# Optimization experiments

Hardware: AMD Instinct MI355X
Metric: run time of the kernel (lower is better)

## Reference

```python
import jax, jax.numpy as jnp
import numpy as np

B, N, M, D, V = 16, 2048, 2048, 128, 128


def setup_inputs() -> dict:
    key0 = jax.random.key(0)
    kq, kk, kv, kp = jax.random.split(key0, 4)
    return {
        "query": jax.random.normal(kq, (B, N, D), dtype=jnp.float32),
        "key": jax.random.normal(kk, (B, M, D), dtype=jnp.float32),
        "value": jax.random.normal(kv, (B, M, V), dtype=jnp.float32),
        "key_padding_len": jax.random.randint(kp, (B,), 0, 512),
        "is_attn_mask_len": 1,  # Python int -> causal masking on
    }


def reference(query, key, value, key_padding_len, is_attn_mask_len):
    # query:[B,N,D], key:[B,M,D], value:[B,M,V], key_padding_len:[B]
    Bq, Nq, Dq = query.shape
    Mk = key.shape[1]
    scale = 1.0 / jnp.sqrt(jnp.asarray(Dq, dtype=query.dtype))

    # torch mask(): zero out the LAST key_padding_len key positions
    pos = jnp.arange(Mk)
    keep = pos[None, :] < (Mk - key_padding_len)[:, None]  # [B,M]
    key = jnp.where(keep[:, :, None], key, jnp.zeros((), key.dtype))

    score = jnp.einsum("bnd,bmd->bnm", query, key) * scale  # [B,N,M]

    if is_attn_mask_len:
        # attn_mask_len[b,i] = M-1-i  ->  row i keeps positions j <= i (causal)
        causal = pos[None, :] <= jnp.arange(Nq)[:, None]  # [N,M]
        score = jnp.where(causal[None, :, :], score, jnp.asarray(-1e6, score.dtype))

    attn = jax.nn.softmax(score, axis=-1)  # dropout p=0 -> identity
    out = jnp.einsum("bnm,bmv->bnv", attn, value)  # [B,N,V]
    return out
```

## Files before the change

### kernel.cpp

```cpp
#include <hip/hip_runtime.h>
#include <stdint.h>

typedef unsigned short ushort_t;
typedef __attribute__((ext_vector_type(8))) short short8;
typedef __attribute__((ext_vector_type(4))) float floatx4;

#define SEQ_N 2048
#define SEQ_M 2048
#define DIM_D 128
#define DIM_V 128
#define BC 64
#define BC2 32


#if __has_builtin(__builtin_amdgcn_exp2f)
#define EXP2F(x) __builtin_amdgcn_exp2f(x)
#else
#define EXP2F(x) exp2f(x)
#endif

template <int CTRL>
__device__ __forceinline__ float dpp_f(float x) {
  int xi = __builtin_bit_cast(int, x);
  int yi = __builtin_amdgcn_update_dpp(xi, xi, CTRL, 0xf, 0xf, false);
  return __builtin_bit_cast(float, yi);
}
__device__ __forceinline__ float rowmax16(float x) {
  x = fmaxf(x, dpp_f<0x128>(x));
  x = fmaxf(x, dpp_f<0x124>(x));
  x = fmaxf(x, dpp_f<0x122>(x));
  x = fmaxf(x, dpp_f<0x121>(x));
  return x;
}
__device__ __forceinline__ float rowsum16(float x) {
  x += dpp_f<0x128>(x);
  x += dpp_f<0x124>(x);
  x += dpp_f<0x122>(x);
  x += dpp_f<0x121>(x);
  return x;
}

__device__ __forceinline__ ushort_t f2bf(float f) {
  uint32_t u = __builtin_bit_cast(uint32_t, f);
  return (ushort_t)((u + 0x8000u) >> 16);
}
__device__ __forceinline__ uint32_t bfpack(float lo, float hi) {
  uint32_t a = __builtin_bit_cast(uint32_t, lo) + 0x8000u;
  uint32_t b = __builtin_bit_cast(uint32_t, hi) + 0x8000u;
  return __builtin_amdgcn_perm(b, a, 0x07060302u);
}

#define K2OFF 0
#define V2OFF 8192
#define P2OFF 16384
#define SMEM2 18432
#define KELEMS 4096
#define VELEMS 4096

#define WS2_KB 0
#define WS2_VT 2097152
#define WS2_PO 4194304
#define WS2_M  8388608
#define WS2_L  8454144
#define WS2_FLOATS 8519680

__device__ __forceinline__ void stage16(const ushort_t* src, ushort_t* lds_base, int lane) {
#if __has_builtin(__builtin_amdgcn_global_load_lds)
  __builtin_amdgcn_global_load_lds(
      (const __attribute__((address_space(1))) void*)src,
      (__attribute__((address_space(3))) void*)lds_base, 16, 0, 0);
#else
  *(uint4*)(lds_base + lane * 8) = *(const uint4*)src;
#endif
}

__global__ __launch_bounds__(256)
void prep2(const float* __restrict__ K, const float* __restrict__ Vg,
           const int* __restrict__ kpl, float* __restrict__ ws) {
  __shared__ __align__(16) ushort_t lt[64][72];
  ushort_t* Kb = (ushort_t*)(ws + WS2_KB);
  ushort_t* Vt = (ushort_t*)(ws + WS2_VT);
  const int g = blockIdx.x, tid = threadIdx.x;
  if (g < 2048) {
    const size_t e = (size_t)g * 2048 + (size_t)tid * 8;
    const int row = (int)(e >> 7);
    const int b = row >> 11, mm = row & 2047;
    const int mlimit = SEQ_M - kpl[b];
    uint4 kw = make_uint4(0u, 0u, 0u, 0u);
    if (mm < mlimit) {
      const float* p = K + e;
      float4 f0 = *(const float4*)p, f1 = *(const float4*)(p + 4);
      kw.x = bfpack(f0.x, f0.y); kw.y = bfpack(f0.z, f0.w);
      kw.z = bfpack(f1.x, f1.y); kw.w = bfpack(f1.z, f1.w);
    }
    *(uint4*)(Kb + e) = kw;
  } else {
    const int g2 = g - 2048;
    const int b = g2 >> 6;
    const int mt = (g2 & 63) >> 1;
    const int vh = (g2 & 1) * 64;
    const int mrow = tid >> 2, v0 = (tid & 3) * 16;
    const float* p = Vg + ((size_t)b * SEQ_M + (size_t)(mt * 64 + mrow)) * DIM_V + vh + v0;
    float4 f0 = *(const float4*)p, f1 = *(const float4*)(p + 4);
    float4 f2 = *(const float4*)(p + 8), f3 = *(const float4*)(p + 12);
    lt[v0 +  0][mrow] = f2bf(f0.x); lt[v0 +  1][mrow] = f2bf(f0.y);
    lt[v0 +  2][mrow] = f2bf(f0.z); lt[v0 +  3][mrow] = f2bf(f0.w);
    lt[v0 +  4][mrow] = f2bf(f1.x); lt[v0 +  5][mrow] = f2bf(f1.y);
    lt[v0 +  6][mrow] = f2bf(f1.z); lt[v0 +  7][mrow] = f2bf(f1.w);
    lt[v0 +  8][mrow] = f2bf(f2.x); lt[v0 +  9][mrow] = f2bf(f2.y);
    lt[v0 + 10][mrow] = f2bf(f2.z); lt[v0 + 11][mrow] = f2bf(f2.w);
    lt[v0 + 12][mrow] = f2bf(f3.x); lt[v0 + 13][mrow] = f2bf(f3.y);
    lt[v0 + 14][mrow] = f2bf(f3.z); lt[v0 + 15][mrow] = f2bf(f3.w);
    __syncthreads();
    const int v = tid >> 2, mo = (tid & 3) * 16;
    ushort_t* dst = Vt + ((size_t)(b * DIM_V + vh + v) * SEQ_M) + mt * 64 + mo;
    *(uint4*)(dst + 0) = *(const uint4*)&lt[v][mo];
    *(uint4*)(dst + 8) = *(const uint4*)&lt[v][mo + 8];
  }
}

__global__ __launch_bounds__(256, 4)
void fa2(const float* __restrict__ Q, const int* __restrict__ amask,
         float* __restrict__ Out, float* __restrict__ ws) {
  __shared__ __align__(16) ushort_t sm[SMEM2];
  const ushort_t* __restrict__ Kb = (const ushort_t*)(ws + WS2_KB);
  const ushort_t* __restrict__ Vt = (const ushort_t*)(ws + WS2_VT);

  const int tid = threadIdx.x;
  const int lane = tid & 63;
  const int w = tid >> 6;
  const int qd = lane >> 4;
  const int nn = lane & 15;

  const int bx = blockIdx.x;
  const int xcd = bx & 7;
  const int q8 = bx >> 3;
  const int s  = q8 >> 5;
  const int v  = q8 & 31;
  const int p  = v & 1;
  const int j  = v >> 1;
  const int b  = xcd * 2 + p;
  const int jj = p ? (15 - j) : j;
  int rt, c;
  if (s == 0)      { rt = jj;      c = 0; }
  else if (s == 1) { rt = 31 - jj; c = 0; }
  else if (s == 2) { rt = 16 + jj; c = 1; }
  else             { rt = 15 - jj; c = 1; }

  const int flag = amask[0];
  const int ntf = flag ? (2 * rt + 2) : (SEQ_M / BC2);
  const int sp  = flag ? (rt + 1) : (SEQ_M / BC2 / 2);
  const int jt_lo = c ? sp : 0;
  const int jt_hi = c ? ntf : sp;

  const int i0w = rt * 64 + w * 16;
  const float c1 = 0.08838834764831845f * 1.4426950408889634f;

  short8 qf[4];
  {
    const float* Qb = Q + ((size_t)b * SEQ_N + (size_t)(i0w + nn)) * DIM_D;
    union { short8 v; uint32_t u32[4]; } tq;
#pragma unroll
    for (int ks = 0; ks < 4; ++ks) {
      const float* pq = Qb + ks * 32 + qd * 8;
      float4 f0 = *(const float4*)pq, f1 = *(const float4*)(pq + 4);
      tq.u32[0] = bfpack(f0.x, f0.y);
      tq.u32[1] = bfpack(f0.z, f0.w);
      tq.u32[2] = bfpack(f1.x, f1.y);
      tq.u32[3] = bfpack(f1.z, f1.w);
      qf[ks] = tq.v;
    }
  }

  floatx4 o[8];
#pragma unroll
  for (int vt = 0; vt < 8; ++vt) o[vt] = (floatx4)0.0f;
  float m[4], l[4];
#pragma unroll
  for (int r = 0; r < 4; ++r) { m[r] = -3.0e38f; l[r] = 0.0f; }

  const size_t kbatch = (size_t)b * (SEQ_M * DIM_D);
  const size_t vbatch = (size_t)b * ((size_t)DIM_V * SEQ_M);

  auto stage = [&](int buf, int jt) {
    const int jb = jt * BC2;
#pragma unroll
    for (int i = 0; i < 2; ++i) {
      const int seg = w * 2 + i;
      {
        const int rrow = seg * 4 + (lane >> 4);
        const int col  = ((lane & 15) * 8) ^ ((rrow & 7) << 3);
        const ushort_t* src = Kb + kbatch + ((size_t)(jb + rrow) << 7) + col;
        stage16(src, &sm[K2OFF + buf * KELEMS + seg * 512], lane);
      }
      {
        const int vrow = seg * 16 + (lane >> 2);
        const int colg = (lane & 3) ^ ((lane >> 4) & 3);
        const ushort_t* src = Vt + vbatch + ((size_t)vrow << 11) + jb + colg * 8;
        stage16(src, &sm[V2OFF + buf * VELEMS + seg * 512], lane);
      }
    }
  };

  stage(0, jt_lo);
  __syncthreads();

  const int len = jt_hi - jt_lo;
  const int swl = (nn & 7) << 3;
  const int vsw = ((nn >> 2) & 3) << 3;
#pragma unroll 1
  for (int t = 0; t < len; ++t) {
    const int cur = t & 1;
    const int jbase = (jt_lo + t) * BC2;
    if (t + 1 < len) stage(cur ^ 1, jt_lo + t + 1);

    const int kb = K2OFF + cur * KELEMS;
    const int vb = V2OFF + cur * VELEMS;

    floatx4 sx[2];
#pragma unroll
    for (int ct = 0; ct < 2; ++ct) sx[ct] = (floatx4)0.0f;
    __builtin_amdgcn_s_setprio(1);
#pragma unroll
    for (int ks = 0; ks < 4; ++ks) {
#pragma unroll
      for (int ct = 0; ct < 2; ++ct) {
        short8 bf = *(const short8*)&sm[kb + (ct * 16 + nn) * 128
                                        + ((ks * 32 + qd * 8) ^ swl)];
        sx[ct] = __builtin_amdgcn_mfma_f32_16x16x32_bf16(qf[ks], bf, sx[ct], 0, 0, 0);
      }
    }
    __builtin_amdgcn_s_setprio(0);

    {
      const bool needmask = flag && (jbase + BC2 - 1 > i0w);
      if (needmask) {
#pragma unroll
        for (int ct = 0; ct < 2; ++ct) {
          const int jgl = jbase + ct * 16 + nn;
#pragma unroll
          for (int r = 0; r < 4; ++r) {
            float tv = sx[ct][r] * c1;
            sx[ct][r] = (jgl > i0w + qd * 4 + r) ? -3.0e38f : tv;
          }
        }
      } else {
#pragma unroll
        for (int ct = 0; ct < 2; ++ct)
#pragma unroll
          for (int r = 0; r < 4; ++r) sx[ct][r] *= c1;
      }
      float mr4[4];
#pragma unroll
      for (int r = 0; r < 4; ++r) mr4[r] = rowmax16(fmaxf(sx[0][r], sx[1][r]));
      bool need = false;
#pragma unroll
      for (int r = 0; r < 4; ++r) need = need || (mr4[r] > m[r] + 8.0f);
      if (__any(need ? 1 : 0)) {
#pragma unroll
        for (int r = 0; r < 4; ++r) {
          const float mn = fmaxf(m[r], mr4[r]);
          const float alpha = EXP2F(m[r] - mn);
          m[r] = mn;
          l[r] *= alpha;
#pragma unroll
          for (int vt = 0; vt < 8; ++vt) o[vt][r] *= alpha;
        }
      }
#pragma unroll
      for (int r = 0; r < 4; ++r) {
        const int prow = w * 16 + qd * 4 + r;
        float p0 = EXP2F(sx[0][r] - m[r]);
        float p1 = EXP2F(sx[1][r] - m[r]);
        l[r] += p0 + p1;
        sm[P2OFF + prow * 32 + ((0 * 16 + nn) ^ (qd << 3))] = f2bf(p0);
        sm[P2OFF + prow * 32 + ((1 * 16 + nn) ^ (qd << 3))] = f2bf(p1);
      }
    }

    __builtin_amdgcn_s_setprio(1);
    {
      short8 a = *(const short8*)&sm[P2OFF + (w * 16 + nn) * 32 + ((qd * 8) ^ vsw)];
#pragma unroll
      for (int vt = 0; vt < 8; ++vt) {
        short8 vbf = *(const short8*)&sm[vb + (vt * 16 + nn) * 32 + ((qd * 8) ^ vsw)];
        o[vt] = __builtin_amdgcn_mfma_f32_16x16x32_bf16(a, vbf, o[vt], 0, 0, 0);
      }
    }
    __builtin_amdgcn_s_setprio(0);

    __syncthreads();
  }

#pragma unroll
  for (int r = 0; r < 4; ++r) l[r] = rowsum16(l[r]);

  const int rb = b * 32 + rt;
  if (c == 0) {
    float* Od = Out + ((size_t)b * SEQ_N + i0w) * DIM_V;
#pragma unroll
    for (int r = 0; r < 4; ++r) {
      const int row = qd * 4 + r;
#pragma unroll
      for (int vt = 0; vt < 8; ++vt)
        Od[(size_t)row * DIM_V + vt * 16 + nn] = o[vt][r];
    }
  } else {
    float* Od = ws + WS2_PO + (size_t)rb * (64 * DIM_V);
#pragma unroll
    for (int r = 0; r < 4; ++r) {
      const int row = w * 16 + qd * 4 + r;
#pragma unroll
      for (int vt = 0; vt < 8; ++vt)
        Od[(size_t)row * DIM_V + vt * 16 + nn] = o[vt][r];
    }
  }
  if (nn == 0) {
    const int slot = rb * 2 + c;
#pragma unroll
    for (int r = 0; r < 4; ++r) {
      const int row = w * 16 + qd * 4 + r;
      ws[WS2_M + slot * 64 + row] = m[r];
      ws[WS2_L + slot * 64 + row] = l[r];
    }
  }
}

__global__ __launch_bounds__(256)
void fa2_merge(float* __restrict__ Out, const float* __restrict__ ws) {
  const int w = threadIdx.x >> 6, lane = threadIdx.x & 63;
  const int rowid = blockIdx.x * 4 + w;
  const int rb = rowid >> 6, rr = rowid & 63;
  const int b = rb >> 5, rt = rb & 31;
  const float m1 = ws[WS2_M + (rb * 2 + 0) * 64 + rr];
  const float l1 = ws[WS2_L + (rb * 2 + 0) * 64 + rr];
  const float m2 = ws[WS2_M + (rb * 2 + 1) * 64 + rr];
  const float l2 = ws[WS2_L + (rb * 2 + 1) * 64 + rr];
  const float M = fmaxf(m1, m2);
  const float a1 = EXP2F(m1 - M), a2 = EXP2F(m2 - M);
  const float inv = 1.0f / (l1 * a1 + l2 * a2);
  float* O1 = Out + ((size_t)b * SEQ_N + (size_t)rt * 64 + rr) * DIM_V;
  const float* O2 = ws + WS2_PO + (size_t)rb * (64 * DIM_V) + (size_t)rr * DIM_V;
  float2 x1 = *(const float2*)(O1 + lane * 2);
  float2 x2 = *(const float2*)(O2 + lane * 2);
  float2 r;
  r.x = (x1.x * a1 + x2.x * a2) * inv;
  r.y = (x1.y * a1 + x2.y * a2) * inv;
  *(float2*)(O1 + lane * 2) = r;
}


#define KS_LD 136
#define VS_LD 72
#define PS_LD 72
#define KB(i) ((i) * 8704)
#define VB(i) (17408 + (i) * 9216)
#define P0 35840
#define SMEM_ELEMS 40448

#define WS_O_FLOATS (256 * 2 * 64 * 128)
#define WS_M_OFF    WS_O_FLOATS
#define WS_L_OFF    (WS_O_FLOATS + 32768)
#define WS_FLOATS   (WS_O_FLOATS + 65536)

__device__ __forceinline__ void process_chunk(
    const float* __restrict__ Q, const float* __restrict__ K,
    const float* __restrict__ Vg, float* __restrict__ Out,
    float* __restrict__ ws, ushort_t* __restrict__ smem,
    int b, int rt, int jt_lo, int jt_hi, int mlimit, int flag, int c, bool direct) {
  const int tid  = threadIdx.x;
  const int lane = tid & 63;
  const int w    = tid >> 6;
  const int qd   = lane >> 4;
  const int nn   = lane & 15;

  const float c1 = 0.08838834764831845f * 1.4426950408889634f;

  const int oct = tid & 15;
  const int j0  = (tid >> 4) * 4;
  const int hh  = nn >> 3;
  const int rb  = 8 * hh;
// ... 227 lines not shown
  r.y = (x1.y * a1 + x2.y * a2) * inv;
  *(float2*)(Out + ((size_t)b * SEQ_N + rt * 64 + rr) * 128 + lane * 2) = r;
}

__global__ __launch_bounds__(256, 2)
void fa_paired(const float* __restrict__ Q, const float* __restrict__ K,
               const float* __restrict__ Vg, const int* __restrict__ kpl,
               const int* __restrict__ amask, float* __restrict__ Out) {
  __shared__ __align__(16) ushort_t smem[SMEM_ELEMS];
  const int bx = blockIdx.x;
  const int b  = bx & 15;
  const int pp = bx >> 4;
  const int flag   = amask[0];
  const int mlimit = SEQ_M - kpl[b];
#pragma unroll 1
  for (int ph = 0; ph < 2; ++ph) {
    const int rt = ph ? (31 - pp) : pp;
    const int ntiles = flag ? (rt + 1) : (SEQ_M / BC);
    process_chunk(Q, K, Vg, Out, nullptr, smem, b, rt, 0, ntiles, mlimit, flag, 0, true);
  }
}

extern "C" void kernel_launch(void* const* d_in, const int* in_sizes, int n_in,
                              void* d_out, int out_size, void* d_ws, size_t ws_size,
                              hipStream_t stream) {
  const float* Q   = (const float*)d_in[0];
  const float* K   = (const float*)d_in[1];
  const float* V   = (const float*)d_in[2];
  const int* kpl   = (const int*)d_in[3];
  const int* amask = (const int*)d_in[4];
  float* O         = (float*)d_out;
  float* ws        = (float*)d_ws;

  if (ws_size >= (size_t)WS2_FLOATS * 4) {
    hipLaunchKernelGGL(prep2, dim3(3072), dim3(256), 0, stream, K, V, kpl, ws);
    hipLaunchKernelGGL(fa2, dim3(1024), dim3(256), 0, stream, Q, amask, O, ws);
    hipLaunchKernelGGL(fa2_merge, dim3(8192), dim3(256), 0, stream, O, ws);
  } else if (ws_size >= (size_t)WS_FLOATS * 4) {
    hipLaunchKernelGGL(fa_chunk, dim3(768), dim3(256), 0, stream, Q, K, V, kpl, amask, O, ws);
    hipLaunchKernelGGL(fa_merge, dim3(4096), dim3(256), 0, stream, ws, O);
  } else {
    hipLaunchKernelGGL(fa_paired, dim3(256), dim3(256), 0, stream, Q, K, V, kpl, amask, O);
  }
}
```

Measured before the change: 151.0 us.

## Fuse K bf16 conversion into attention kernel and split causal rows into variable chunks

Removes the K fp32->bf16 pre-pass from the prep kernel. The attention kernel now loads fp32 K into registers, converts it and applies the padding mask, then writes it to swizzled LDS, with the LDS write deferred until after the compute of the current tile. The causal work split changes from two chunks per row tile to 1–4 chunks depending on row length, giving 1248 blocks. The merge kernel is generalised to combine up to four partials. This trades more fp32 K traffic and in-kernel conversion work for one less pass over K and better load balance.

```diff
diff --git a/kernel.cpp b/kernel.cpp
--- a/kernel.cpp
+++ b/kernel.cpp
@@ -57,11 +57,10 @@
 #define KELEMS 4096
 #define VELEMS 4096
 
-#define WS2_KB 0
-#define WS2_VT 2097152
-#define WS2_PO 4194304
-#define WS2_M  8388608
-#define WS2_L  8454144
+#define WS2_VT 0
+#define WS2_PO 2097152
+#define WS2_M  8126464
+#define WS2_L  8206336
 #define WS2_FLOATS 8519680
 
 __device__ __forceinline__ void stage16(const ushort_t* src, ushort_t* lds_base, int lane) {
@@ -75,55 +74,51 @@
 }
 
 __global__ __launch_bounds__(256)
-void prep2(const float* __restrict__ K, const float* __restrict__ Vg,
-           const int* __restrict__ kpl, float* __restrict__ ws) {
+void prep2(const float* __restrict__ Vg, float* __restrict__ ws) {
   __shared__ __align__(16) ushort_t lt[64][72];
-  ushort_t* Kb = (ushort_t*)(ws + WS2_KB);
   ushort_t* Vt = (ushort_t*)(ws + WS2_VT);
   const int g = blockIdx.x, tid = threadIdx.x;
-  if (g < 2048) {
-    const size_t e = (size_t)g * 2048 + (size_t)tid * 8;
-    const int row = (int)(e >> 7);
-    const int b = row >> 11, mm = row & 2047;
-    const int mlimit = SEQ_M - kpl[b];
-    uint4 kw = make_uint4(0u, 0u, 0u, 0u);
-    if (mm < mlimit) {
-      const float* p = K + e;
-      float4 f0 = *(const float4*)p, f1 = *(const float4*)(p + 4);
-      kw.x = bfpack(f0.x, f0.y); kw.y = bfpack(f0.z, f0.w);
-      kw.z = bfpack(f1.x, f1.y); kw.w = bfpack(f1.z, f1.w);
-    }
-    *(uint4*)(Kb + e) = kw;
-  } else {
-    const int g2 = g - 2048;
-    const int b = g2 >> 6;
-    const int mt = (g2 & 63) >> 1;
-    const int vh = (g2 & 1) * 64;
-    const int mrow = tid >> 2, v0 = (tid & 3) * 16;
-    const float* p = Vg + ((size_t)b * SEQ_M + (size_t)(mt * 64 + mrow)) * DIM_V + vh + v0;
-    float4 f0 = *(const float4*)p, f1 = *(const float4*)(p + 4);
-    float4 f2 = *(const float4*)(p + 8), f3 = *(const float4*)(p + 12);
-    lt[v0 +  0][mrow] = f2bf(f0.x); lt[v0 +  1][mrow] = f2bf(f0.y);
-    lt[v0 +  2][mrow] = f2bf(f0.z); lt[v0 +  3][mrow] = f2bf(f0.w);
-    lt[v0 +  4][mrow] = f2bf(f1.x); lt[v0 +  5][mrow] = f2bf(f1.y);
-    lt[v0 +  6][mrow] = f2bf(f1.z); lt[v0 +  7][mrow] = f2bf(f1.w);
-    lt[v0 +  8][mrow] = f2bf(f2.x); lt[v0 +  9][mrow] = f2bf(f2.y);
-    lt[v0 + 10][mrow] = f2bf(f2.z); lt[v0 + 11][mrow] = f2bf(f2.w);
-    lt[v0 + 12][mrow] = f2bf(f3.x); lt[v0 + 13][mrow] = f2bf(f3.y);
-    lt[v0 + 14][mrow] = f2bf(f3.z); lt[v0 + 15][mrow] = f2bf(f3.w);
-    __syncthreads();
-    const int v = tid >> 2, mo = (tid & 3) * 16;
-    ushort_t* dst = Vt + ((size_t)(b * DIM_V + vh + v) * SEQ_M) + mt * 64 + mo;
-    *(uint4*)(dst + 0) = *(const uint4*)&lt[v][mo];
-    *(uint4*)(dst + 8) = *(const uint4*)&lt[v][mo + 8];
-  }
+  const int b = g >> 6;
+  const int mt = (g & 63) >> 1;
+  const int vh = (g & 1) * 64;
+  const int mrow = tid >> 2, v0 = (tid & 3) * 16;
+  const float* p = Vg + ((size_t)b * SEQ_M + (size_t)(mt * 64 + mrow)) * DIM_V + vh + v0;
+  float4 f0 = *(const float4*)p, f1 = *(const float4*)(p + 4);
+  float4 f2 = *(const float4*)(p + 8), f3 = *(const float4*)(p + 12);
+  lt[v0 +  0][mrow] = f2bf(f0.x); lt[v0 +  1][mrow] = f2bf(f0.y);
+  lt[v0 +  2][mrow] = f2bf(f0.z); lt[v0 +  3][mrow] = f2bf(f0.w);
+  lt[v0 +  4][mrow] = f2bf(f1.x); lt[v0 +  5][mrow] = f2bf(f1.y);
+  lt[v0 +  6][mrow] = f2bf(f1.z); lt[v0 +  7][mrow] = f2bf(f1.w);
+  lt[v0 +  8][mrow] = f2bf(f2.x); lt[v0 +  9][mrow] = f2bf(f2.y);
+  lt[v0 + 10][mrow] = f2bf(f2.z); lt[v0 + 11][mrow] = f2bf(f2.w);
+  lt[v0 + 12][mrow] = f2bf(f3.x); lt[v0 + 13][mrow] = f2bf(f3.y);
+  lt[v0 + 14][mrow] = f2bf(f3.z); lt[v0 + 15][mrow] = f2bf(f3.w);
+  __syncthreads();
+  const int v = tid >> 2, mo = (tid & 3) * 16;
+  ushort_t* dst = Vt + ((size_t)(b * DIM_V + vh + v) * SEQ_M) + mt * 64 + mo;
+  *(uint4*)(dst + 0) = *(const uint4*)&lt[v][mo];
+  *(uint4*)(dst + 8) = *(const uint4*)&lt[v][mo + 8];
+}
+
+__device__ __forceinline__ int nch_of(int rt) {
+  return (rt <= 7) ? 1 : ((rt <= 16) ? 2 : ((rt <= 24) ? 3 : 4));
+}
+__device__ __forceinline__ int cbase_of(int rt) {
+  return (rt <= 7) ? rt
+       : ((rt <= 16) ? (8 + 2 * (rt - 8))
+       : ((rt <= 24) ? (26 + 3 * (rt - 17)) : (50 + 4 * (rt - 25))));
+}
+__device__ __forceinline__ int sbase_of(int rt) {
+  return (rt <= 7) ? 0
+       : ((rt <= 16) ? (rt - 8)
+       : ((rt <= 24) ? (9 + 2 * (rt - 17)) : (25 + 3 * (rt - 25))));
 }
 
 __global__ __launch_bounds__(256, 4)
-void fa2(const float* __restrict__ Q, const int* __restrict__ amask,
+void fa2(const float* __restrict__ Q, const float* __restrict__ Kg,
+         const int* __restrict__ kpl, const int* __restrict__ amask,
          float* __restrict__ Out, float* __restrict__ ws) {
   __shared__ __align__(16) ushort_t sm[SMEM2];
-  const ushort_t* __restrict__ Kb = (const ushort_t*)(ws + WS2_KB);
   const ushort_t* __restrict__ Vt = (const ushort_t*)(ws + WS2_VT);
 
   const int tid = threadIdx.x;
@@ -134,25 +129,27 @@
 
   const int bx = blockIdx.x;
   const int xcd = bx & 7;
-  const int q8 = bx >> 3;
-  const int s  = q8 >> 5;
-  const int v  = q8 & 31;
-  const int p  = v & 1;
-  const int j  = v >> 1;
-  const int b  = xcd * 2 + p;
-  const int jj = p ? (15 - j) : j;
-  int rt, c;
-  if (s == 0)      { rt = jj;      c = 0; }
-  else if (s == 1) { rt = 31 - jj; c = 0; }
-  else if (s == 2) { rt = 16 + jj; c = 1; }
-  else             { rt = 15 - jj; c = 1; }
-
+  const int q = bx >> 3;
+  const int b = xcd * 2 + (q & 1);
+  const int idx = q >> 1;
   const int flag = amask[0];
+
+  int rt, c, nch;
+  if (flag) {
+    if (idx < 28)      { rt = 31 - (idx >> 2); c = idx & 3; }
+    else if (idx < 52) { int i = idx - 28; int d = i / 3; rt = 24 - d; c = i - 3 * d; }
+    else if (idx < 70) { int i = idx - 52; rt = 16 - (i >> 1); c = i & 1; }
+    else               { rt = 77 - idx; c = 0; }
+    nch = nch_of(rt);
+  } else {
+    if (idx >= 64) return;
+    rt = idx >> 1; c = idx & 1; nch = 2;
+  }
   const int ntf = flag ? (2 * rt + 2) : (SEQ_M / BC2);
-  const int sp  = flag ? (rt + 1) : (SEQ_M / BC2 / 2);
-  const int jt_lo = c ? sp : 0;
-  const int jt_hi = c ? ntf : sp;
-
+  const int jt_lo = (ntf * c) / nch;
+  const int jt_hi = (ntf * (c + 1)) / nch;
+
+  const int mlimit = SEQ_M - kpl[b];
   const int i0w = rt * 64 + w * 16;
   const float c1 = 0.08838834764831845f * 1.4426950408889634f;
 
@@ -179,30 +176,47 @@
 #pragma unroll
   for (int r = 0; r < 4; ++r) { m[r] = -3.0e38f; l[r] = 0.0f; }
 
-  const size_t kbatch = (size_t)b * (SEQ_M * DIM_D);
+  const size_t kgoff = (size_t)b * (SEQ_M * DIM_D);
   const size_t vbatch = (size_t)b * ((size_t)DIM_V * SEQ_M);
 
-  auto stage = [&](int buf, int jt) {
+  const int kr_row = tid >> 3;
+  const int kcg    = tid & 7;
+  float4 kr[4];
+  auto kload = [&](int jt) {
+    const float* p = Kg + kgoff + ((size_t)(jt * BC2 + kr_row) << 7) + kcg * 16;
+    kr[0] = *(const float4*)p;       kr[1] = *(const float4*)(p + 4);
+    kr[2] = *(const float4*)(p + 8); kr[3] = *(const float4*)(p + 12);
+  };
+  auto kwrite = [&](int buf, int jt) {
+    uint4 w0, w1;
+    w0.x = bfpack(kr[0].x, kr[0].y); w0.y = bfpack(kr[0].z, kr[0].w);
+    w0.z = bfpack(kr[1].x, kr[1].y); w0.w = bfpack(kr[1].z, kr[1].w);
+    w1.x = bfpack(kr[2].x, kr[2].y); w1.y = bfpack(kr[2].z, kr[2].w);
+    w1.z = bfpack(kr[3].x, kr[3].y); w1.w = bfpack(kr[3].z, kr[3].w);
+    if (jt * BC2 + kr_row >= mlimit) {
+      w0 = make_uint4(0u, 0u, 0u, 0u);
+      w1 = make_uint4(0u, 0u, 0u, 0u);
+    }
+    ushort_t* kb = &sm[K2OFF + buf * KELEMS + kr_row * 128];
+    const int g0 = kcg * 2;
+    *(uint4*)(kb + (((g0 + 0) ^ (kr_row & 7)) << 3)) = w0;
+    *(uint4*)(kb + (((g0 + 1) ^ (kr_row & 7)) << 3)) = w1;
+  };
+  auto stage_v = [&](int buf, int jt) {
     const int jb = jt * BC2;
 #pragma unroll
     for (int i = 0; i < 2; ++i) {
       const int seg = w * 2 + i;
-      {
-        const int rrow = seg * 4 + (lane >> 4);
-        const int col  = ((lane & 15) * 8) ^ ((rrow & 7) << 3);
-        const ushort_t* src = Kb + kbatch + ((size_t)(jb + rrow) << 7) + col;
-        stage16(src, &sm[K2OFF + buf * KELEMS + seg * 512], lane);
-      }
-      {
-        const int vrow = seg * 16 + (lane >> 2);
-        const int colg = (lane & 3) ^ ((lane >> 4) & 3);
-        const ushort_t* src = Vt + vbatch + ((size_t)vrow << 11) + jb + colg * 8;
-        stage16(src, &sm[V2OFF + buf * VELEMS + seg * 512], lane);
-      }
+      const int vrow = seg * 16 + (lane >> 2);
+      const int colg = (lane & 3) ^ ((lane >> 4) & 3);
+      const ushort_t* src = Vt + vbatch + ((size_t)vrow << 11) + jb + colg * 8;
+      stage16(src, &sm[V2OFF + buf * VELEMS + seg * 512], lane);
     }
   };
 
-  stage(0, jt_lo);
+  kload(jt_lo);
+  stage_v(0, jt_lo);
+  kwrite(0, jt_lo);
   __syncthreads();
 
   const int len = jt_hi - jt_lo;
@@ -211,8 +225,10 @@
 #pragma unroll 1
   for (int t = 0; t < len; ++t) {
     const int cur = t & 1;
-    const int jbase = (jt_lo + t) * BC2;
-    if (t + 1 < len) stage(cur ^ 1, jt_lo + t + 1);
+    const int jt = jt_lo + t;
+    const bool more = (t + 1) < len;
+    const int jbase = jt * BC2;
+    if (more) { kload(jt + 1); stage_v(cur ^ 1, jt + 1); }
 
     const int kb = K2OFF + cur * KELEMS;
     const int vb = V2OFF + cur * VELEMS;
@@ -289,13 +305,14 @@
     }
     __builtin_amdgcn_s_setprio(0);
 
+    if (more) kwrite(cur ^ 1, jt + 1);
     __syncthreads();
   }
 
 #pragma unroll
   for (int r = 0; r < 4; ++r) l[r] = rowsum16(l[r]);
 
-  const int rb = b * 32 + rt;
+  const int cid = b * 78 + (flag ? (cbase_of(rt) + c) : (rt * 2 + c));
   if (c == 0) {
     float* Od = Out + ((size_t)b * SEQ_N + i0w) * DIM_V;
 #pragma unroll
@@ -306,7 +323,8 @@
         Od[(size_t)row * DIM_V + vt * 16 + nn] = o[vt][r];
     }
   } else {
-    float* Od = ws + WS2_PO + (size_t)rb * (64 * DIM_V);
+    const int slot = flag ? (b * 46 + sbase_of(rt) + (c - 1)) : (b * 32 + rt);
+    float* Od = ws + WS2_PO + (size_t)slot * (64 * DIM_V);
 #pragma unroll
     for (int r = 0; r < 4; ++r) {
       const int row = w * 16 + qd * 4 + r;
@@ -316,37 +334,61 @@
     }
   }
   if (nn == 0) {
-    const int slot = rb * 2 + c;
 #pragma unroll
     for (int r = 0; r < 4; ++r) {
       const int row = w * 16 + qd * 4 + r;
-      ws[WS2_M + slot * 64 + row] = m[r];
-      ws[WS2_L + slot * 64 + row] = l[r];
+      ws[WS2_M + cid * 64 + row] = m[r];
+      ws[WS2_L + cid * 64 + row] = l[r];
     }
   }
 }
 
 __global__ __launch_bounds__(256)
-void fa2_merge(float* __restrict__ Out, const float* __restrict__ ws) {
+void fa2_merge(float* __restrict__ Out, const float* __restrict__ ws,
+               const int* __restrict__ amask) {
   const int w = threadIdx.x >> 6, lane = threadIdx.x & 63;
   const int rowid = blockIdx.x * 4 + w;
-  const int rb = rowid >> 6, rr = rowid & 63;
-  const int b = rb >> 5, rt = rb & 31;
-  const float m1 = ws[WS2_M + (rb * 2 + 0) * 64 + rr];
-  const float l1 = ws[WS2_L + (rb * 2 + 0) * 64 + rr];
-  const float m2 = ws[WS2_M + (rb * 2 + 1) * 64 + rr];
-  const float l2 = ws[WS2_L + (rb * 2 + 1) * 64 + rr];
-  const float M = fmaxf(m1, m2);
-  const float a1 = EXP2F(m1 - M), a2 = EXP2F(m2 - M);
-  const float inv = 1.0f / (l1 * a1 + l2 * a2);
-  float* O1 = Out + ((size_t)b * SEQ_N + (size_t)rt * 64 + rr) * DIM_V;
-  const float* O2 = ws + WS2_PO + (size_t)rb * (64 * DIM_V) + (size_t)rr * DIM_V;
-  float2 x1 = *(const float2*)(O1 + lane * 2);
-  float2 x2 = *(const float2*)(O2 + lane * 2);
-  float2 r;
-  r.x = (x1.x * a1 + x2.x * a2) * inv;
-  r.y = (x1.y * a1 + x2.y * a2) * inv;
-  *(float2*)(O1 + lane * 2) = r;
+  const int b = rowid >> 11;
+  const int gr = rowid & 2047;
+  const int rt = gr >> 6, rr = gr & 63;
+  const int flag = amask[0];
+  int nch, cb, sb;
+  if (flag) { nch = nch_of(rt); cb = cbase_of(rt); sb = sbase_of(rt); }
+  else      { nch = 2; cb = rt * 2; sb = 0; }
+  const int cid0 = b * 78 + cb;
+
+  float m0 = ws[WS2_M + (cid0 + 0) * 64 + rr];
+  float l0 = ws[WS2_L + (cid0 + 0) * 64 + rr];
+  float m1 = -3.0e38f, l1 = 0.0f, m2 = -3.0e38f, l2 = 0.0f, m3 = -3.0e38f, l3 = 0.0f;
+  if (nch > 1) { m1 = ws[WS2_M + (cid0 + 1) * 64 + rr]; l1 = ws[WS2_L + (cid0 + 1) * 64 + rr]; }
+  if (nch > 2) { m2 = ws[WS2_M + (cid0 + 2) * 64 + rr]; l2 = ws[WS2_L + (cid0 + 2) * 64 + rr]; }
+  if (nch > 3) { m3 = ws[WS2_M + (cid0 + 3) * 64 + rr]; l3 = ws[WS2_L + (cid0 + 3) * 64 + rr]; }
+  const float M = fmaxf(fmaxf(m0, m1), fmaxf(m2, m3));
+  const float e0 = EXP2F(m0 - M), e1 = EXP2F(m1 - M);
+  const float e2 = EXP2F(m2 - M), e3 = EXP2F(m3 - M);
+  const float inv = 1.0f / (l0 * e0 + l1 * e1 + l2 * e2 + l3 * e3);
+
+  float* O1 = Out + ((size_t)b * SEQ_N + gr) * DIM_V;
+  float2 x = *(const float2*)(O1 + lane * 2);
+  const float a0 = e0 * inv;
+  float2 acc; acc.x = x.x * a0; acc.y = x.y * a0;
+  const int slotb = flag ? (b * 46 + sb) : (b * 32 + rt);
+  if (nch > 1) {
+    const float* P = ws + WS2_PO + (size_t)(slotb + 0) * (64 * DIM_V) + rr * DIM_V;
+    float2 y = *(const float2*)(P + lane * 2);
+    const float a1 = e1 * inv; acc.x += y.x * a1; acc.y += y.y * a1;
+  }
+  if (nch > 2) {
+    const float* P = ws + WS2_PO + (size_t)(slotb + 1) * (64 * DIM_V) + rr * DIM_V;
+    float2 y = *(const float2*)(P + lane * 2);
+    const float a2 = e2 * inv; acc.x += y.x * a2; acc.y += y.y * a2;
+  }
+  if (nch > 3) {
+    const float* P = ws + WS2_PO + (size_t)(slotb + 2) * (64 * DIM_V) + rr * DIM_V;
+    float2 y = *(const float2*)(P + lane * 2);
+    const float a3 = e3 * inv; acc.x += y.x * a3; acc.y += y.y * a3;
+  }
+  *(float2*)(O1 + lane * 2) = acc;
 }
 
 
@@ -641,9 +683,9 @@
   float* ws        = (float*)d_ws;
 
   if (ws_size >= (size_t)WS2_FLOATS * 4) {
-    hipLaunchKernelGGL(prep2, dim3(3072), dim3(256), 0, stream, K, V, kpl, ws);
-    hipLaunchKernelGGL(fa2, dim3(1024), dim3(256), 0, stream, Q, amask, O, ws);
-    hipLaunchKernelGGL(fa2_merge, dim3(8192), dim3(256), 0, stream, O, ws);
+    hipLaunchKernelGGL(prep2, dim3(1024), dim3(256), 0, stream, V, ws);
+    hipLaunchKernelGGL(fa2, dim3(1248), dim3(256), 0, stream, Q, K, kpl, amask, O, ws);
+    hipLaunchKernelGGL(fa2_merge, dim3(8192), dim3(256), 0, stream, O, ws, amask);
   } else if (ws_size >= (size_t)WS_FLOATS * 4) {
     hipLaunchKernelGGL(fa_chunk, dim3(768), dim3(256), 0, stream, Q, K, V, kpl, amask, O, ws);
     hipLaunchKernelGGL(fa_merge, dim3(4096), dim3(256), 0, stream, ws, O);
```

Result: slower. 163.7 us (+8.4%).

## Split causal row tiles into variable key-chunk counts to balance work

Applied to the files above, without the earlier changes.

Replaces the fixed two-way key split per row tile with a variable number of chunks (up to 3 or 4) chosen by row position, so long causal rows are spread over more blocks. Work items are ordered longest-first, and the merge kernel now combines up to four partial results using per-chunk max and sum. Which mode runs depends on workspace size. The aim is to cut tail imbalance across CUs, at the cost of more partial-output traffic and a heavier merge.

```diff
diff --git a/kernel.cpp b/kernel.cpp
--- a/kernel.cpp
+++ b/kernel.cpp
@@ -60,9 +60,6 @@
 #define WS2_KB 0
 #define WS2_VT 2097152
 #define WS2_PO 4194304
-#define WS2_M  8388608
-#define WS2_L  8454144
-#define WS2_FLOATS 8519680
 
 __device__ __forceinline__ void stage16(const ushort_t* src, ushort_t* lds_base, int lane) {
 #if __has_builtin(__builtin_amdgcn_global_load_lds)
@@ -119,9 +116,32 @@
   }
 }
 
+__device__ __forceinline__ int nch_m1(int rt) { return (rt <= 7) ? 1 : ((rt <= 21) ? 2 : 3); }
+__device__ __forceinline__ int cb_m1(int rt) {
+  return (rt <= 7) ? rt : ((rt <= 21) ? (8 + 2 * (rt - 8)) : (36 + 3 * (rt - 22)));
+}
+__device__ __forceinline__ int sb_m1(int rt) {
+  return (rt <= 7) ? 0 : ((rt <= 21) ? (rt - 8) : (14 + 2 * (rt - 22)));
+}
+__device__ __forceinline__ int nch_m2(int rt) {
+  return (rt <= 7) ? 1 : ((rt <= 16) ? 2 : ((rt <= 24) ? 3 : 4));
+}
+__device__ __forceinline__ int cb_m2(int rt) {
+  return (rt <= 7) ? rt
+       : ((rt <= 16) ? (8 + 2 * (rt - 8))
+       : ((rt <= 24) ? (26 + 3 * (rt - 17)) : (50 + 4 * (rt - 25))));
+}
+__device__ __forceinline__ int sb_m2(int rt) {
+  return (rt <= 7) ? 0
+       : ((rt <= 16) ? (rt - 8)
+       : ((rt <= 24) ? (9 + 2 * (rt - 17)) : (25 + 3 * (rt - 25))));
+}
+
 __global__ __launch_bounds__(256, 4)
 void fa2(const float* __restrict__ Q, const int* __restrict__ amask,
-         float* __restrict__ Out, float* __restrict__ ws) {
+         float* __restrict__ Out, float* __restrict__ ws,
+         float* __restrict__ PO, float* __restrict__ MP, float* __restrict__ LP,
+         int mode) {
   __shared__ __align__(16) ushort_t sm[SMEM2];
   const ushort_t* __restrict__ Kb = (const ushort_t*)(ws + WS2_KB);
   const ushort_t* __restrict__ Vt = (const ushort_t*)(ws + WS2_VT);
@@ -134,24 +154,44 @@
 
   const int bx = blockIdx.x;
   const int xcd = bx & 7;
-  const int q8 = bx >> 3;
-  const int s  = q8 >> 5;
-  const int v  = q8 & 31;
-  const int p  = v & 1;
-  const int j  = v >> 1;
-  const int b  = xcd * 2 + p;
-  const int jj = p ? (15 - j) : j;
-  int rt, c;
-  if (s == 0)      { rt = jj;      c = 0; }
-  else if (s == 1) { rt = 31 - jj; c = 0; }
-  else if (s == 2) { rt = 16 + jj; c = 1; }
-  else             { rt = 15 - jj; c = 1; }
-
+  const int q = bx >> 3;
   const int flag = amask[0];
+
+  int b, rt, c, nch;
+  if (mode == 0) {
+    const int s = q >> 5, v5 = q & 31, pz = v5 & 1, j = v5 >> 1;
+    b = xcd * 2 + pz;
+    const int jj = pz ? (15 - j) : j;
+    if (s == 0)      { rt = jj;      c = 0; }
+    else if (s == 1) { rt = 31 - jj; c = 0; }
+    else if (s == 2) { rt = 16 + jj; c = 1; }
+    else             { rt = 15 - jj; c = 1; }
+    nch = 2;
+  } else {
+    b = xcd * 2 + (q & 1);
+    const int idx = q >> 1;
+    if (flag) {
+      if (mode == 1) {
+        if (idx < 30)      { const int d = idx / 3; rt = 31 - d; c = idx - 3 * d; }
+        else if (idx < 58) { const int i = idx - 30; rt = 21 - (i >> 1); c = i & 1; }
+        else               { rt = 65 - idx; c = 0; }
+        nch = nch_m1(rt);
+      } else {
+        if (idx < 28)      { rt = 31 - (idx >> 2); c = idx & 3; }
+        else if (idx < 52) { const int i = idx - 28; const int d = i / 3; rt = 24 - d; c = i - 3 * d; }
+        else if (idx < 70) { const int i = idx - 52; rt = 16 - (i >> 1); c = i & 1; }
+        else               { rt = 77 - idx; c = 0; }
+        nch = nch_m2(rt);
+      }
+    } else {
+      if (idx >= 64) return;
+      rt = idx >> 1; c = idx & 1; nch = 2;
+    }
+  }
+
   const int ntf = flag ? (2 * rt + 2) : (SEQ_M / BC2);
-  const int sp  = flag ? (rt + 1) : (SEQ_M / BC2 / 2);
-  const int jt_lo = c ? sp : 0;
-  const int jt_hi = c ? ntf : sp;
+  const int jt_lo = (ntf * c) / nch;
+  const int jt_hi = (ntf * (c + 1)) / nch;
 
   const int i0w = rt * 64 + w * 16;
   const float c1 = 0.08838834764831845f * 1.4426950408889634f;
@@ -295,7 +335,13 @@
 #pragma unroll
   for (int r = 0; r < 4; ++r) l[r] = rowsum16(l[r]);
 
-  const int rb = b * 32 + rt;
+  int cid, slotb;
+  if (mode == 0)      { cid = (b * 32 + rt) * 2 + c; slotb = b * 32 + rt; }
+  else if (mode == 1) { cid = b * 66 + (flag ? cb_m1(rt) : rt * 2) + c;
+                        slotb = b * 34 + (flag ? sb_m1(rt) : rt); }
+  else                { cid = b * 78 + (flag ? cb_m2(rt) : rt * 2) + c;
+                        slotb = b * 46 + (flag ? sb_m2(rt) : rt); }
+
   if (c == 0) {
     float* Od = Out + ((size_t)b * SEQ_N + i0w) * DIM_V;
 #pragma unroll
@@ -306,7 +352,7 @@
         Od[(size_t)row * DIM_V + vt * 16 + nn] = o[vt][r];
     }
   } else {
-    float* Od = ws + WS2_PO + (size_t)rb * (64 * DIM_V);
+    float* Od = PO + (size_t)(slotb + c - 1) * (64 * DIM_V);
 #pragma unroll
     for (int r = 0; r < 4; ++r) {
       const int row = w * 16 + qd * 4 + r;
@@ -316,37 +362,67 @@
     }
   }
   if (nn == 0) {
-    const int slot = rb * 2 + c;
 #pragma unroll
     for (int r = 0; r < 4; ++r) {
       const int row = w * 16 + qd * 4 + r;
-      ws[WS2_M + slot * 64 + row] = m[r];
-      ws[WS2_L + slot * 64 + row] = l[r];
+      MP[cid * 64 + row] = m[r];
+      LP[cid * 64 + row] = l[r];
     }
   }
 }
 
 __global__ __launch_bounds__(256)
-void fa2_merge(float* __restrict__ Out, const float* __restrict__ ws) {
+void fa2_merge(float* __restrict__ Out, const float* __restrict__ PO,
+               const float* __restrict__ MP, const float* __restrict__ LP,
+               const int* __restrict__ amask, int mode) {
   const int w = threadIdx.x >> 6, lane = threadIdx.x & 63;
   const int rowid = blockIdx.x * 4 + w;
-  const int rb = rowid >> 6, rr = rowid & 63;
-  const int b = rb >> 5, rt = rb & 31;
-  const float m1 = ws[WS2_M + (rb * 2 + 0) * 64 + rr];
-  const float l1 = ws[WS2_L + (rb * 2 + 0) * 64 + rr];
-  const float m2 = ws[WS2_M + (rb * 2 + 1) * 64 + rr];
-  const float l2 = ws[WS2_L + (rb * 2 + 1) * 64 + rr];
-  const float M = fmaxf(m1, m2);
-  const float a1 = EXP2F(m1 - M), a2 = EXP2F(m2 - M);
-  const float inv = 1.0f / (l1 * a1 + l2 * a2);
-  float* O1 = Out + ((size_t)b * SEQ_N + (size_t)rt * 64 + rr) * DIM_V;
-  const float* O2 = ws + WS2_PO + (size_t)rb * (64 * DIM_V) + (size_t)rr * DIM_V;
-  float2 x1 = *(const float2*)(O1 + lane * 2);
-  float2 x2 = *(const float2*)(O2 + lane * 2);
-  float2 r;
-  r.x = (x1.x * a1 + x2.x * a2) * inv;
-  r.y = (x1.y * a1 + x2.y * a2) * inv;
-  *(float2*)(O1 + lane * 2) = r;
+  const int b = rowid >> 11;
+  const int gr = rowid & 2047;
+  const int rt = gr >> 6, rr = gr & 63;
+  const int flag = amask[0];
+
+  int nch, cid0, slotb;
+  if (mode == 0)      { nch = 2; cid0 = (b * 32 + rt) * 2; slotb = b * 32 + rt; }
+  else if (mode == 1) {
+    if (flag) { nch = nch_m1(rt); cid0 = b * 66 + cb_m1(rt); slotb = b * 34 + sb_m1(rt); }
+    else      { nch = 2; cid0 = b * 66 + rt * 2; slotb = b * 34 + rt; }
+  } else {
+    if (flag) { nch = nch_m2(rt); cid0 = b * 78 + cb_m2(rt); slotb = b * 46 + sb_m2(rt); }
+    else      { nch = 2; cid0 = b * 78 + rt * 2; slotb = b * 46 + rt; }
+  }
+
+  float m0 = MP[(cid0 + 0) * 64 + rr];
+  float l0 = LP[(cid0 + 0) * 64 + rr];
+  float m1 = -3.0e38f, l1 = 0.0f, m2 = -3.0e38f, l2 = 0.0f, m3 = -3.0e38f, l3 = 0.0f;
+  if (nch > 1) { m1 = MP[(cid0 + 1) * 64 + rr]; l1 = LP[(cid0 + 1) * 64 + rr]; }
+  if (nch > 2) { m2 = MP[(cid0 + 2) * 64 + rr]; l2 = LP[(cid0 + 2) * 64 + rr]; }
+  if (nch > 3) { m3 = MP[(cid0 + 3) * 64 + rr]; l3 = LP[(cid0 + 3) * 64 + rr]; }
+  const float M = fmaxf(fmaxf(m0, m1), fmaxf(m2, m3));
+  const float e0 = EXP2F(m0 - M), e1 = EXP2F(m1 - M);
+  const float e2 = EXP2F(m2 - M), e3 = EXP2F(m3 - M);
+  const float inv = 1.0f / (l0 * e0 + l1 * e1 + l2 * e2 + l3 * e3);
+
+  float* O1 = Out + ((size_t)b * SEQ_N + gr) * DIM_V;
+  float2 x = *(const float2*)(O1 + lane * 2);
+  const float a0 = e0 * inv;
+  float2 acc; acc.x = x.x * a0; acc.y = x.y * a0;
+  if (nch > 1) {
+    const float* P = PO + (size_t)(slotb + 0) * (64 * DIM_V) + rr * DIM_V;
+    float2 y = *(const float2*)(P + lane * 2);
+    const float a1 = e1 * inv; acc.x += y.x * a1; acc.y += y.y * a1;
+  }
+  if (nch > 2) {
+    const float* P = PO + (size_t)(slotb + 1) * (64 * DIM_V) + rr * DIM_V;
+    float2 y = *(const float2*)(P + lane * 2);
+    const float a2 = e2 * inv; acc.x += y.x * a2; acc.y += y.y * a2;
+  }
+  if (nch > 3) {
+    const float* P = PO + (size_t)(slotb + 2) * (64 * DIM_V) + rr * DIM_V;
+    float2 y = *(const float2*)(P + lane * 2);
+    const float a3 = e3 * inv; acc.x += y.x * a3; acc.y += y.y * a3;
+  }
+  *(float2*)(O1 + lane * 2) = acc;
 }
 
 
@@ -640,10 +716,20 @@
   float* O         = (float*)d_out;
   float* ws        = (float*)d_ws;
 
-  if (ws_size >= (size_t)WS2_FLOATS * 4) {
+  int mode = -1;
+  int grid = 0;
+  size_t mloff = 0, lloff = 0;
+  if (ws_size >= 41533440ull)      { mode = 2; grid = 1248; mloff = 10223616; lloff = 10303488; }
+  else if (ws_size >= 35143680ull) { mode = 1; grid = 1056; mloff = 8650752;  lloff = 8718336;  }
+  else if (ws_size >= 34078720ull) { mode = 0; grid = 1024; mloff = 8388608;  lloff = 8454144;  }
+
+  if (mode >= 0) {
+    float* PO = ws + WS2_PO;
+    float* MP = ws + mloff;
+    float* LP = ws + lloff;
     hipLaunchKernelGGL(prep2, dim3(3072), dim3(256), 0, stream, K, V, kpl, ws);
-    hipLaunchKernelGGL(fa2, dim3(1024), dim3(256), 0, stream, Q, amask, O, ws);
-    hipLaunchKernelGGL(fa2_merge, dim3(8192), dim3(256), 0, stream, O, ws);
+    hipLaunchKernelGGL(fa2, dim3(grid), dim3(256), 0, stream, Q, amask, O, ws, PO, MP, LP, mode);
+    hipLaunchKernelGGL(fa2_merge, dim3(8192), dim3(256), 0, stream, O, PO, MP, LP, amask, mode);
   } else if (ws_size >= (size_t)WS_FLOATS * 4) {
     hipLaunchKernelGGL(fa_chunk, dim3(768), dim3(256), 0, stream, Q, K, V, kpl, amask, O, ws);
     hipLaunchKernelGGL(fa_merge, dim3(4096), dim3(256), 0, stream, ws, O);
```

Result: no change. 153.9 us (+1.9%).

## Compute transposed S=K·Q^T so P stays in registers, dropping LDS round-trip

Applied to the files above, without the earlier changes.

Swaps the MFMA operand order in the score product so each lane holds one query's scores for a column of keys. The softmax probabilities are then packed directly into the A-operand register fragment for the PV MFMA, which removes the P write/read through shared memory and shrinks the LDS allocation. To make this register layout line up with V, the V-transpose prep kernel permutes key positions within each 64-key tile. Row max and sum become per-lane scalars reduced with two shuffles, and the per-row output rescale factor is fetched by shuffle. Correctness now depends on the key permutation in prep matching the MFMA register layout exactly.

```diff
diff --git a/kernel.cpp b/kernel.cpp
--- a/kernel.cpp
+++ b/kernel.cpp
@@ -52,8 +52,7 @@
 
 #define K2OFF 0
 #define V2OFF 8192
-#define P2OFF 16384
-#define SMEM2 18432
+#define SMEM2 16384
 #define KELEMS 4096
 #define VELEMS 4096
 
@@ -100,17 +99,20 @@
     const int mt = (g2 & 63) >> 1;
     const int vh = (g2 & 1) * 64;
     const int mrow = tid >> 2, v0 = (tid & 3) * 16;
+    const int pm = mrow & 31;
+    const int mcol = (mrow & 32) + (((pm >> 2) & 3) << 3)
+                   + (((pm >> 4) & 1) << 2) + (pm & 3);
     const float* p = Vg + ((size_t)b * SEQ_M + (size_t)(mt * 64 + mrow)) * DIM_V + vh + v0;
     float4 f0 = *(const float4*)p, f1 = *(const float4*)(p + 4);
     float4 f2 = *(const float4*)(p + 8), f3 = *(const float4*)(p + 12);
-    lt[v0 +  0][mrow] = f2bf(f0.x); lt[v0 +  1][mrow] = f2bf(f0.y);
-    lt[v0 +  2][mrow] = f2bf(f0.z); lt[v0 +  3][mrow] = f2bf(f0.w);
-    lt[v0 +  4][mrow] = f2bf(f1.x); lt[v0 +  5][mrow] = f2bf(f1.y);
-    lt[v0 +  6][mrow] = f2bf(f1.z); lt[v0 +  7][mrow] = f2bf(f1.w);
-    lt[v0 +  8][mrow] = f2bf(f2.x); lt[v0 +  9][mrow] = f2bf(f2.y);
-    lt[v0 + 10][mrow] = f2bf(f2.z); lt[v0 + 11][mrow] = f2bf(f2.w);
-    lt[v0 + 12][mrow] = f2bf(f3.x); lt[v0 + 13][mrow] = f2bf(f3.y);
-    lt[v0 + 14][mrow] = f2bf(f3.z); lt[v0 + 15][mrow] = f2bf(f3.w);
+    lt[v0 +  0][mcol] = f2bf(f0.x); lt[v0 +  1][mcol] = f2bf(f0.y);
+    lt[v0 +  2][mcol] = f2bf(f0.z); lt[v0 +  3][mcol] = f2bf(f0.w);
+    lt[v0 +  4][mcol] = f2bf(f1.x); lt[v0 +  5][mcol] = f2bf(f1.y);
+    lt[v0 +  6][mcol] = f2bf(f1.z); lt[v0 +  7][mcol] = f2bf(f1.w);
+    lt[v0 +  8][mcol] = f2bf(f2.x); lt[v0 +  9][mcol] = f2bf(f2.y);
+    lt[v0 + 10][mcol] = f2bf(f2.z); lt[v0 + 11][mcol] = f2bf(f2.w);
+    lt[v0 + 12][mcol] = f2bf(f3.x); lt[v0 + 13][mcol] = f2bf(f3.y);
+    lt[v0 + 14][mcol] = f2bf(f3.z); lt[v0 + 15][mcol] = f2bf(f3.w);
     __syncthreads();
     const int v = tid >> 2, mo = (tid & 3) * 16;
     ushort_t* dst = Vt + ((size_t)(b * DIM_V + vh + v) * SEQ_M) + mt * 64 + mo;
@@ -121,7 +123,8 @@
 
 __global__ __launch_bounds__(256, 4)
 void fa2(const float* __restrict__ Q, const int* __restrict__ amask,
-         float* __restrict__ Out, float* __restrict__ ws) {
+         float* __restrict__ Out, float* __restrict__ ws,
+         float* __restrict__ PO, float* __restrict__ MP, float* __restrict__ LP) {
   __shared__ __align__(16) ushort_t sm[SMEM2];
   const ushort_t* __restrict__ Kb = (const ushort_t*)(ws + WS2_KB);
   const ushort_t* __restrict__ Vt = (const ushort_t*)(ws + WS2_VT);
@@ -134,31 +137,30 @@
 
   const int bx = blockIdx.x;
   const int xcd = bx & 7;
-  const int q8 = bx >> 3;
-  const int s  = q8 >> 5;
-  const int v  = q8 & 31;
-  const int p  = v & 1;
-  const int j  = v >> 1;
-  const int b  = xcd * 2 + p;
-  const int jj = p ? (15 - j) : j;
+  const int q = bx >> 3;
+  const int flag = amask[0];
+
+  const int s = q >> 5, v5 = q & 31, pz = v5 & 1, j = v5 >> 1;
+  const int b = xcd * 2 + pz;
+  const int jj = pz ? (15 - j) : j;
   int rt, c;
   if (s == 0)      { rt = jj;      c = 0; }
   else if (s == 1) { rt = 31 - jj; c = 0; }
   else if (s == 2) { rt = 16 + jj; c = 1; }
   else             { rt = 15 - jj; c = 1; }
 
-  const int flag = amask[0];
   const int ntf = flag ? (2 * rt + 2) : (SEQ_M / BC2);
   const int sp  = flag ? (rt + 1) : (SEQ_M / BC2 / 2);
   const int jt_lo = c ? sp : 0;
   const int jt_hi = c ? ntf : sp;
 
   const int i0w = rt * 64 + w * 16;
+  const int qgl = i0w + nn;
   const float c1 = 0.08838834764831845f * 1.4426950408889634f;
 
   short8 qf[4];
   {
-    const float* Qb = Q + ((size_t)b * SEQ_N + (size_t)(i0w + nn)) * DIM_D;
+    const float* Qb = Q + ((size_t)b * SEQ_N + (size_t)qgl) * DIM_D;
     union { short8 v; uint32_t u32[4]; } tq;
 #pragma unroll
     for (int ks = 0; ks < 4; ++ks) {
@@ -175,9 +177,10 @@
   floatx4 o[8];
 #pragma unroll
   for (int vt = 0; vt < 8; ++vt) o[vt] = (floatx4)0.0f;
-  float m[4], l[4];
-#pragma unroll
-  for (int r = 0; r < 4; ++r) { m[r] = -3.0e38f; l[r] = 0.0f; }
+  float m = -3.0e38f, l = 0.0f;
+  float m_o[4];
+#pragma unroll
+  for (int r = 0; r < 4; ++r) m_o[r] = -3.0e38f;
 
   const size_t kbatch = (size_t)b * (SEQ_M * DIM_D);
   const size_t vbatch = (size_t)b * ((size_t)DIM_V * SEQ_M);
@@ -225,77 +228,79 @@
     for (int ks = 0; ks < 4; ++ks) {
 #pragma unroll
       for (int ct = 0; ct < 2; ++ct) {
-        short8 bf = *(const short8*)&sm[kb + (ct * 16 + nn) * 128
+        short8 kf = *(const short8*)&sm[kb + (ct * 16 + nn) * 128
                                         + ((ks * 32 + qd * 8) ^ swl)];
-        sx[ct] = __builtin_amdgcn_mfma_f32_16x16x32_bf16(qf[ks], bf, sx[ct], 0, 0, 0);
+        sx[ct] = __builtin_amdgcn_mfma_f32_16x16x32_bf16(kf, qf[ks], sx[ct], 0, 0, 0);
       }
     }
     __builtin_amdgcn_s_setprio(0);
 
-    {
-      const bool needmask = flag && (jbase + BC2 - 1 > i0w);
-      if (needmask) {
-#pragma unroll
-        for (int ct = 0; ct < 2; ++ct) {
-          const int jgl = jbase + ct * 16 + nn;
-#pragma unroll
-          for (int r = 0; r < 4; ++r) {
-            float tv = sx[ct][r] * c1;
-            sx[ct][r] = (jgl > i0w + qd * 4 + r) ? -3.0e38f : tv;
-          }
+    const bool needmask = flag && (jbase + BC2 - 1 > i0w);
+    if (needmask) {
+#pragma unroll
+      for (int ct = 0; ct < 2; ++ct) {
+        const int kbase = jbase + ct * 16 + qd * 4 - qgl;
+#pragma unroll
+        for (int r = 0; r < 4; ++r) {
+          const float tv = sx[ct][r] * c1;
+          sx[ct][r] = (kbase + r > 0) ? -3.0e38f : tv;
         }
-      } else {
-#pragma unroll
-        for (int ct = 0; ct < 2; ++ct)
-#pragma unroll
-          for (int r = 0; r < 4; ++r) sx[ct][r] *= c1;
-      }
-      float mr4[4];
-#pragma unroll
-      for (int r = 0; r < 4; ++r) mr4[r] = rowmax16(fmaxf(sx[0][r], sx[1][r]));
-      bool need = false;
-#pragma unroll
-      for (int r = 0; r < 4; ++r) need = need || (mr4[r] > m[r] + 8.0f);
-      if (__any(need ? 1 : 0)) {
-#pragma unroll
-        for (int r = 0; r < 4; ++r) {
-          const float mn = fmaxf(m[r], mr4[r]);
-          const float alpha = EXP2F(m[r] - mn);
-          m[r] = mn;
-          l[r] *= alpha;
-#pragma unroll
-          for (int vt = 0; vt < 8; ++vt) o[vt][r] *= alpha;
-        }
-      }
+      }
+    } else {
+#pragma unroll
+      for (int ct = 0; ct < 2; ++ct)
+#pragma unroll
+        for (int r = 0; r < 4; ++r) sx[ct][r] *= c1;
+    }
+    float mr = fmaxf(fmaxf(fmaxf(sx[0][0], sx[0][1]), fmaxf(sx[0][2], sx[0][3])),
+                     fmaxf(fmaxf(sx[1][0], sx[1][1]), fmaxf(sx[1][2], sx[1][3])));
+    mr = fmaxf(mr, __shfl_xor(mr, 16));
+    mr = fmaxf(mr, __shfl_xor(mr, 32));
+
+    if (__any((mr > m + 8.0f) ? 1 : 0)) {
+      const float mn = fmaxf(m, mr);
+      l *= EXP2F(m - mn);
+      m = mn;
 #pragma unroll
       for (int r = 0; r < 4; ++r) {
-        const int prow = w * 16 + qd * 4 + r;
-        float p0 = EXP2F(sx[0][r] - m[r]);
-        float p1 = EXP2F(sx[1][r] - m[r]);
-        l[r] += p0 + p1;
-        sm[P2OFF + prow * 32 + ((0 * 16 + nn) ^ (qd << 3))] = f2bf(p0);
-        sm[P2OFF + prow * 32 + ((1 * 16 + nn) ^ (qd << 3))] = f2bf(p1);
-      }
-    }
+        const float mo_n = __shfl(mn, (qd << 4) + qd * 4 + r);
+        const float al = EXP2F(m_o[r] - mo_n);
+        m_o[r] = mo_n;
+#pragma unroll
+        for (int vt = 0; vt < 8; ++vt) o[vt][r] *= al;
+      }
+    }
+
+    float p[2][4];
+#pragma unroll
+    for (int ct = 0; ct < 2; ++ct)
+#pragma unroll
+      for (int r = 0; r < 4; ++r) {
+        p[ct][r] = EXP2F(sx[ct][r] - m);
+        l += p[ct][r];
+      }
+    union { short8 v; uint32_t u[4]; } pa;
+    pa.u[0] = bfpack(p[0][0], p[0][1]);
+    pa.u[1] = bfpack(p[0][2], p[0][3]);
+    pa.u[2] = bfpack(p[1][0], p[1][1]);
+    pa.u[3] = bfpack(p[1][2], p[1][3]);
 
     __builtin_amdgcn_s_setprio(1);
-    {
-      short8 a = *(const short8*)&sm[P2OFF + (w * 16 + nn) * 32 + ((qd * 8) ^ vsw)];
-#pragma unroll
-      for (int vt = 0; vt < 8; ++vt) {
-        short8 vbf = *(const short8*)&sm[vb + (vt * 16 + nn) * 32 + ((qd * 8) ^ vsw)];
-        o[vt] = __builtin_amdgcn_mfma_f32_16x16x32_bf16(a, vbf, o[vt], 0, 0, 0);
-      }
+#pragma unroll
+    for (int vt = 0; vt < 8; ++vt) {
+      short8 vbf = *(const short8*)&sm[vb + (vt * 16 + nn) * 32 + ((qd * 8) ^ vsw)];
+      o[vt] = __builtin_amdgcn_mfma_f32_16x16x32_bf16(pa.v, vbf, o[vt], 0, 0, 0);
     }
     __builtin_amdgcn_s_setprio(0);
 
     __syncthreads();
   }
 
-#pragma unroll
-  for (int r = 0; r < 4; ++r) l[r] = rowsum16(l[r]);
-
-  const int rb = b * 32 + rt;
+  l += __shfl_xor(l, 16);
+  l += __shfl_xor(l, 32);
+
+  const int cid = (b * 32 + rt) * 2 + c;
+  const int slotb = b * 32 + rt;
   if (c == 0) {
     float* Od = Out + ((size_t)b * SEQ_N + i0w) * DIM_V;
 #pragma unroll
@@ -306,7 +311,7 @@
         Od[(size_t)row * DIM_V + vt * 16 + nn] = o[vt][r];
     }
   } else {
-    float* Od = ws + WS2_PO + (size_t)rb * (64 * DIM_V);
+    float* Od = PO + (size_t)slotb * (64 * DIM_V);
 #pragma unroll
     for (int r = 0; r < 4; ++r) {
       const int row = w * 16 + qd * 4 + r;
@@ -315,32 +320,28 @@
         Od[(size_t)row * DIM_V + vt * 16 + nn] = o[vt][r];
     }
   }
-  if (nn == 0) {
-    const int slot = rb * 2 + c;
-#pragma unroll
-    for (int r = 0; r < 4; ++r) {
-      const int row = w * 16 + qd * 4 + r;
-      ws[WS2_M + slot * 64 + row] = m[r];
-      ws[WS2_L + slot * 64 + row] = l[r];
-    }
+  if (lane < 16) {
+    MP[cid * 64 + w * 16 + nn] = m;
+    LP[cid * 64 + w * 16 + nn] = l;
   }
 }
 
 __global__ __launch_bounds__(256)
-void fa2_merge(float* __restrict__ Out, const float* __restrict__ ws) {
+void fa2_merge(float* __restrict__ Out, const float* __restrict__ PO,
+               const float* __restrict__ MP, const float* __restrict__ LP) {
   const int w = threadIdx.x >> 6, lane = threadIdx.x & 63;
   const int rowid = blockIdx.x * 4 + w;
   const int rb = rowid >> 6, rr = rowid & 63;
   const int b = rb >> 5, rt = rb & 31;
-  const float m1 = ws[WS2_M + (rb * 2 + 0) * 64 + rr];
-  const float l1 = ws[WS2_L + (rb * 2 + 0) * 64 + rr];
-  const float m2 = ws[WS2_M + (rb * 2 + 1) * 64 + rr];
-  const float l2 = ws[WS2_L + (rb * 2 + 1) * 64 + rr];
+  const float m1 = MP[(rb * 2 + 0) * 64 + rr];
+  const float l1 = LP[(rb * 2 + 0) * 64 + rr];
+  const float m2 = MP[(rb * 2 + 1) * 64 + rr];
+  const float l2 = LP[(rb * 2 + 1) * 64 + rr];
   const float M = fmaxf(m1, m2);
   const float a1 = EXP2F(m1 - M), a2 = EXP2F(m2 - M);
   const float inv = 1.0f / (l1 * a1 + l2 * a2);
   float* O1 = Out + ((size_t)b * SEQ_N + (size_t)rt * 64 + rr) * DIM_V;
-  const float* O2 = ws + WS2_PO + (size_t)rb * (64 * DIM_V) + (size_t)rr * DIM_V;
+  const float* O2 = PO + (size_t)rb * (64 * DIM_V) + (size_t)rr * DIM_V;
   float2 x1 = *(const float2*)(O1 + lane * 2);
   float2 x2 = *(const float2*)(O2 + lane * 2);
   float2 r;
@@ -641,9 +642,12 @@
   float* ws        = (float*)d_ws;
 
   if (ws_size >= (size_t)WS2_FLOATS * 4) {
+    float* PO = ws + WS2_PO;
+    float* MP = ws + WS2_M;
+    float* LP = ws + WS2_L;
     hipLaunchKernelGGL(prep2, dim3(3072), dim3(256), 0, stream, K, V, kpl, ws);
-    hipLaunchKernelGGL(fa2, dim3(1024), dim3(256), 0, stream, Q, amask, O, ws);
-    hipLaunchKernelGGL(fa2_merge, dim3(8192), dim3(256), 0, stream, O, ws);
+    hipLaunchKernelGGL(fa2, dim3(1024), dim3(256), 0, stream, Q, amask, O, ws, PO, MP, LP);
+    hipLaunchKernelGGL(fa2_merge, dim3(8192), dim3(256), 0, stream, O, PO, MP, LP);
   } else if (ws_size >= (size_t)WS_FLOATS * 4) {
     hipLaunchKernelGGL(fa_chunk, dim3(768), dim3(256), 0, stream, Q, K, V, kpl, amask, O, ws);
     hipLaunchKernelGGL(fa_merge, dim3(4096), dim3(256), 0, stream, ws, O);
```

Measured after the change: 143.0 us. 1.06x faster.
